# Kernel optimization log

Hardware: AMD Instinct MI355X
Metric: run time of the kernel (lower is better)

Reference implementation:

```python
import jax, jax.numpy as jnp
import numpy as np

GAMMA = 0.5
BATCH, DIM, UNITS = 16384, 512, 1024


def setup_inputs() -> dict:
    key = jax.random.key(0)
    k1, k2 = jax.random.split(key)
    inputs = jax.random.normal(k1, (BATCH, DIM), dtype=jnp.float32)
    mu = jax.random.normal(k2, (DIM, UNITS), dtype=jnp.float32)
    return {"inputs": inputs, "mu": mu}


def reference(inputs, mu):
    # Squared L2 distance from each input row to each center (column of mu):
    x_sq = jnp.sum(inputs * inputs, axis=1, keepdims=True)        # [B, 1]
    mu_sq = jnp.sum(mu * mu, axis=0, keepdims=True)               # [1, U]
    cross = inputs @ mu                                           # [B, U] GEMM
    l2 = x_sq - 2.0 * cross + mu_sq                                # [B, U]
    return jnp.exp(-GAMMA * l2)
```

## Files before the change

kernel.cpp:

```cpp
#include <hip/hip_runtime.h>
#include <hip/hip_bf16.h>

#define BATCH 16384
#define DIM   512
#define UNITS 1024

typedef float v16f __attribute__((ext_vector_type(16)));

#define APITCH 516
#define BPITCH 33

#define MFMA_F8(a, b, c) __builtin_amdgcn_mfma_f32_32x32x16_fp8_fp8((a), (b), (c), 0, 0, 0)

__device__ __forceinline__ void async_copy16(const void* g, void* l) {
    __builtin_amdgcn_global_load_lds(
        (const __attribute__((address_space(1))) void*)g,
        (__attribute__((address_space(3))) void*)l,
        16 , 0 , 0 );
}

__global__ __launch_bounds__(256)
void prep_kernel(const float* __restrict__ in, const float* __restrict__ mu,
                 unsigned char* __restrict__ A8f, unsigned char* __restrict__ B8f,
                 float* __restrict__ xsq, float* __restrict__ musq) {
    __shared__ __attribute__((aligned(16))) char smem[512 * BPITCH * 4 + 1024];
    const int t  = threadIdx.x;
    const int l  = t & 63, w = t >> 6;
    const int ln = l & 31, h = l >> 5;

    if (blockIdx.x >= UNITS / 32) {
        float* lds = (float*)smem;
        float* red = (float*)(smem + 32 * APITCH * 4);
        const int bb = blockIdx.x - UNITS / 32;
        const int c  = (bb & 7) * 64 + (bb >> 3);
        const float4* src = (const float4*)(in + (size_t)c * 32 * DIM);
        float4* l4 = (float4*)lds;
#pragma unroll
        for (int i = 0; i < 16; i++) {
            const int f = i * 256 + t;
            l4[(f >> 7) * (APITCH / 4) + (f & 127)] = src[f];
        }
        __syncthreads();
        float s = 0.f;
#pragma unroll
        for (int j = 0; j < 8; j++) {
            const int kw = w * 8 + j;
            const float* p = lds + ln * APITCH + kw * 16 + h * 8;
            float4 f0 = *(const float4*)p;
            float4 f1 = *(const float4*)(p + 4);
            s += f0.x * f0.x + f0.y * f0.y + f0.z * f0.z + f0.w * f0.w
               + f1.x * f1.x + f1.y * f1.y + f1.z * f1.z + f1.w * f1.w;
            int lo = __builtin_amdgcn_cvt_pk_fp8_f32(f0.x, f0.y, 0, false);
            lo     = __builtin_amdgcn_cvt_pk_fp8_f32(f0.z, f0.w, lo, true);
            int hi = __builtin_amdgcn_cvt_pk_fp8_f32(f1.x, f1.y, 0, false);
            hi     = __builtin_amdgcn_cvt_pk_fp8_f32(f1.z, f1.w, hi, true);
            *(int2*)(A8f + (((size_t)c * 32 + kw) * 64 + l) * 8) = make_int2(lo, hi);
        }
        red[ln * 8 + w * 2 + h] = s;
        __syncthreads();
        if (t < 32) {
            float a = 0.f;
#pragma unroll
            for (int i = 0; i < 8; i++) a += red[t * 8 + i];
            xsq[c * 32 + t] = a;
        }
    } else {
        float* lds = (float*)smem;
        float* red = (float*)(smem + 512 * BPITCH * 4);
        const int nb = blockIdx.x;
        const int n0 = nb * 32;
        const int col = t & 31, kg = t >> 5;
        float s = 0.f;
        for (int i = 0; i < 64; i++) {
            const int k = i * 8 + kg;
            float v = mu[(size_t)k * UNITS + n0 + col];
            s += v * v;
            lds[k * BPITCH + col] = v;
        }
        red[col * 8 + kg] = s;
        __syncthreads();
        if (t < 32) {
            float a = 0.f;
#pragma unroll
            for (int i = 0; i < 8; i++) a += red[t * 8 + i];
            musq[n0 + t] = a;
        }
#pragma unroll
        for (int j = 0; j < 8; j++) {
            const int kw = w * 8 + j;
            const float* p = lds + (kw * 16 + h * 8) * BPITCH + ln;
            float f[8];
#pragma unroll
            for (int i = 0; i < 8; i++) f[i] = p[i * BPITCH];
            int lo = __builtin_amdgcn_cvt_pk_fp8_f32(f[0], f[1], 0, false);
            lo     = __builtin_amdgcn_cvt_pk_fp8_f32(f[2], f[3], lo, true);
            int hi = __builtin_amdgcn_cvt_pk_fp8_f32(f[4], f[5], 0, false);
            hi     = __builtin_amdgcn_cvt_pk_fp8_f32(f[6], f[7], hi, true);
            *(int2*)(B8f + (((size_t)nb * 32 + kw) * 64 + l) * 8) = make_int2(lo, hi);
        }
    }
}

__global__ __launch_bounds__(256, 4)
void rbf_gemm_kernel(const unsigned char* __restrict__ A8f,
                     const unsigned char* __restrict__ B8f,
                     const float* __restrict__ xsq,
                     const float* __restrict__ musq,
                     float* __restrict__ out) {
    __shared__ __attribute__((aligned(16))) unsigned char Bs[32768];

    const int t  = threadIdx.x;
    const int l  = t & 63;
    const int w  = t >> 6;
    const int ln = l & 31;
    const int h  = l >> 5;

    const int b   = blockIdx.x;
    const int xcd = b & 7;
    const int j   = b >> 3;
    const int m0  = (xcd * 8 + (j & 7)) * 256;
    const int n0  = (j >> 3) * 64;

    const unsigned char* bsrc = B8f + (size_t)n0 * 512;
#pragma unroll
    for (int i = 0; i < 8; i++) {
        const int c = i * 256 + t;
        async_copy16(bsrc + c * 16, Bs + c * 16);
    }
    __syncthreads();

    const long* BsL = (const long*)Bs;
    const long* Bp  = BsL + l;

#pragma unroll
    for (int p = 0; p < 2; p++) {
        const int mbase = m0 + w * 64 + p * 32;
        const long* Af = (const long*)A8f + (size_t)(mbase >> 5) * 2048 + l;

        v16f acc0 = (v16f)0.f, acc1 = (v16f)0.f;
#pragma unroll 4
        for (int kw = 0; kw < 32; kw++) {
            long a  = Af[kw * 64];
            long b0 = Bp[kw * 64];
            long b1 = Bp[2048 + kw * 64];
            acc0 = MFMA_F8(a, b0, acc0);
            acc1 = MFMA_F8(a, b1, acc1);
        }

        const float xv  = -0.5f * xsq[mbase + ln];
        const float mb0 = -0.5f * musq[n0 + ln];
        const float mb1 = -0.5f * musq[n0 + 32 + ln];
        float* obase = out + n0 + ln;
#pragma unroll
        for (int r = 0; r < 16; r++) {
            const int rl = (r & 3) + 8 * (r >> 2) + 4 * h;
            const float xb = __shfl(xv, rl, 64);
            float* orow = obase + (size_t)(mbase + rl) * UNITS;
            __builtin_nontemporal_store(__expf(acc0[r] + xb + mb0), orow);
            __builtin_nontemporal_store(__expf(acc1[r] + xb + mb1), orow + 32);
        }
    }
}

extern "C" void kernel_launch(void* const* d_in, const int* in_sizes, int n_in,
                              void* d_out, int out_size, void* d_ws, size_t ws_size,
                              hipStream_t stream) {
    const float* inputs = (const float*)d_in[0];
    const float* mu     = (const float*)d_in[1];
    float* out = (float*)d_out;

    char* ws = (char*)d_ws;
    unsigned char* A8f = (unsigned char*)ws;
    unsigned char* B8f = (unsigned char*)(ws + (size_t)BATCH * DIM);
    float* xsq  = (float*)(ws + (size_t)BATCH * DIM + (size_t)UNITS * DIM);
    float* musq = xsq + BATCH;

    prep_kernel<<<UNITS / 32 + BATCH / 32, 256, 0, stream>>>(
        inputs, mu, A8f, B8f, xsq, musq);
    rbf_gemm_kernel<<<1024, 256, 0, stream>>>(A8f, B8f, xsq, musq, out);
}
```

Measured before the change: 109.1 us.

## Fuse input fp8 conversion and row norms into the GEMM kernel

The input quantization and row squared-norm computation move out of the prep kernel and into the main GEMM kernel. Each 1024-thread block stages 64 input rows in LDS, converts them to fp8 fragments and reduces the norms locally. The block then computes all 1024 output columns, reading B fragments straight from global/L2 instead of LDS. This removes the A8f/xsq round trip through global memory and shrinks the prep launch. In exchange the kernel uses a large LDS footprint, runs only 256 blocks, and gives up the async B staging and the XCD-aware block mapping.

```diff
diff --git a/kernel.cpp b/kernel.cpp
--- a/kernel.cpp
+++ b/kernel.cpp
@@ -1,5 +1,4 @@
 #include <hip/hip_runtime.h>
-#include <hip/hip_bf16.h>
 
 #define BATCH 16384
 #define DIM   512
@@ -7,155 +6,141 @@
 
 typedef float v16f __attribute__((ext_vector_type(16)));
 
-#define APITCH 516
 #define BPITCH 33
-
 #define MFMA_F8(a, b, c) __builtin_amdgcn_mfma_f32_32x32x16_fp8_fp8((a), (b), (c), 0, 0, 0)
 
-__device__ __forceinline__ void async_copy16(const void* g, void* l) {
-    __builtin_amdgcn_global_load_lds(
-        (const __attribute__((address_space(1))) void*)g,
-        (__attribute__((address_space(3))) void*)l,
-        16 , 0 , 0 );
+static __device__ __forceinline__ int2 cvt8(const float4 f0, const float4 f1) {
+    int lo = __builtin_amdgcn_cvt_pk_fp8_f32(f0.x, f0.y, 0, false);
+    lo     = __builtin_amdgcn_cvt_pk_fp8_f32(f0.z, f0.w, lo, true);
+    int hi = __builtin_amdgcn_cvt_pk_fp8_f32(f1.x, f1.y, 0, false);
+    hi     = __builtin_amdgcn_cvt_pk_fp8_f32(f1.z, f1.w, hi, true);
+    return make_int2(lo, hi);
+}
+static __device__ __forceinline__ float dot8(const float4 f0, const float4 f1) {
+    return f0.x * f0.x + f0.y * f0.y + f0.z * f0.z + f0.w * f0.w
+         + f1.x * f1.x + f1.y * f1.y + f1.z * f1.z + f1.w * f1.w;
 }
 
 __global__ __launch_bounds__(256)
-void prep_kernel(const float* __restrict__ in, const float* __restrict__ mu,
-                 unsigned char* __restrict__ A8f, unsigned char* __restrict__ B8f,
-                 float* __restrict__ xsq, float* __restrict__ musq) {
+void prep_b_kernel(const float* __restrict__ mu, unsigned char* __restrict__ B8f,
+                   float* __restrict__ musq) {
     __shared__ __attribute__((aligned(16))) char smem[512 * BPITCH * 4 + 1024];
+    float* lds = (float*)smem;
+    float* red = (float*)(smem + 512 * BPITCH * 4);
     const int t  = threadIdx.x;
     const int l  = t & 63, w = t >> 6;
     const int ln = l & 31, h = l >> 5;
-
-    if (blockIdx.x >= UNITS / 32) {
-        float* lds = (float*)smem;
-        float* red = (float*)(smem + 32 * APITCH * 4);
-        const int bb = blockIdx.x - UNITS / 32;
-        const int c  = (bb & 7) * 64 + (bb >> 3);
-        const float4* src = (const float4*)(in + (size_t)c * 32 * DIM);
-        float4* l4 = (float4*)lds;
+    const int nb = blockIdx.x;
+    const int n0 = nb * 32;
+    const int col = t & 31, kg = t >> 5;
+    float s = 0.f;
+    for (int i = 0; i < 64; i++) {
+        const int k = i * 8 + kg;
+        float v = mu[(size_t)k * UNITS + n0 + col];
+        s += v * v;
+        lds[k * BPITCH + col] = v;
+    }
+    red[col * 8 + kg] = s;
+    __syncthreads();
+    if (t < 32) {
+        float a = 0.f;
 #pragma unroll
-        for (int i = 0; i < 16; i++) {
-            const int f = i * 256 + t;
-            l4[(f >> 7) * (APITCH / 4) + (f & 127)] = src[f];
-        }
-        __syncthreads();
-        float s = 0.f;
+        for (int i = 0; i < 8; i++) a += red[t * 8 + i];
+        musq[n0 + t] = a;
+    }
 #pragma unroll
-        for (int j = 0; j < 8; j++) {
-            const int kw = w * 8 + j;
-            const float* p = lds + ln * APITCH + kw * 16 + h * 8;
-            float4 f0 = *(const float4*)p;
-            float4 f1 = *(const float4*)(p + 4);
-            s += f0.x * f0.x + f0.y * f0.y + f0.z * f0.z + f0.w * f0.w
-               + f1.x * f1.x + f1.y * f1.y + f1.z * f1.z + f1.w * f1.w;
-            int lo = __builtin_amdgcn_cvt_pk_fp8_f32(f0.x, f0.y, 0, false);
-            lo     = __builtin_amdgcn_cvt_pk_fp8_f32(f0.z, f0.w, lo, true);
-            int hi = __builtin_amdgcn_cvt_pk_fp8_f32(f1.x, f1.y, 0, false);
-            hi     = __builtin_amdgcn_cvt_pk_fp8_f32(f1.z, f1.w, hi, true);
-            *(int2*)(A8f + (((size_t)c * 32 + kw) * 64 + l) * 8) = make_int2(lo, hi);
-        }
-        red[ln * 8 + w * 2 + h] = s;
-        __syncthreads();
-        if (t < 32) {
-            float a = 0.f;
+    for (int j = 0; j < 8; j++) {
+        const int kw = w * 8 + j;
+        const float* p = lds + (kw * 16 + h * 8) * BPITCH + ln;
+        float f[8];
 #pragma unroll
-            for (int i = 0; i < 8; i++) a += red[t * 8 + i];
-            xsq[c * 32 + t] = a;
-        }
-    } else {
-        float* lds = (float*)smem;
-        float* red = (float*)(smem + 512 * BPITCH * 4);
-        const int nb = blockIdx.x;
-        const int n0 = nb * 32;
-        const int col = t & 31, kg = t >> 5;
-        float s = 0.f;
-        for (int i = 0; i < 64; i++) {
-            const int k = i * 8 + kg;
-            float v = mu[(size_t)k * UNITS + n0 + col];
-            s += v * v;
-            lds[k * BPITCH + col] = v;
-        }
-        red[col * 8 + kg] = s;
-        __syncthreads();
-        if (t < 32) {
-            float a = 0.f;
-#pragma unroll
-            for (int i = 0; i < 8; i++) a += red[t * 8 + i];
-            musq[n0 + t] = a;
-        }
-#pragma unroll
-        for (int j = 0; j < 8; j++) {
-            const int kw = w * 8 + j;
-            const float* p = lds + (kw * 16 + h * 8) * BPITCH + ln;
-            float f[8];
-#pragma unroll
-            for (int i = 0; i < 8; i++) f[i] = p[i * BPITCH];
-            int lo = __builtin_amdgcn_cvt_pk_fp8_f32(f[0], f[1], 0, false);
-            lo     = __builtin_amdgcn_cvt_pk_fp8_f32(f[2], f[3], lo, true);
-            int hi = __builtin_amdgcn_cvt_pk_fp8_f32(f[4], f[5], 0, false);
-            hi     = __builtin_amdgcn_cvt_pk_fp8_f32(f[6], f[7], hi, true);
-            *(int2*)(B8f + (((size_t)nb * 32 + kw) * 64 + l) * 8) = make_int2(lo, hi);
-        }
+        for (int i = 0; i < 8; i++) f[i] = p[i * BPITCH];
+        *(int2*)(B8f + (((size_t)nb * 32 + kw) * 64 + l) * 8) =
+            cvt8(make_float4(f[0], f[1], f[2], f[3]),
+                 make_float4(f[4], f[5], f[6], f[7]));
     }
 }
 
-__global__ __launch_bounds__(256, 4)
-void rbf_gemm_kernel(const unsigned char* __restrict__ A8f,
+__global__ __launch_bounds__(1024, 4)
+void rbf_main_kernel(const float* __restrict__ in,
                      const unsigned char* __restrict__ B8f,
-                     const float* __restrict__ xsq,
                      const float* __restrict__ musq,
                      float* __restrict__ out) {
-    __shared__ __attribute__((aligned(16))) unsigned char Bs[32768];
+    __shared__ __attribute__((aligned(16))) unsigned char smem[107520];
+    float* stage = (float*)smem;
+    unsigned char* Afrag = smem + 66048;
+    float* red   = (float*)(smem + 98816);
+    float* xsq_l = (float*)(smem + 107264);
 
     const int t  = threadIdx.x;
     const int l  = t & 63;
     const int w  = t >> 6;
     const int ln = l & 31;
     const int h  = l >> 5;
+    const int m0 = blockIdx.x * 64;
 
-    const int b   = blockIdx.x;
-    const int xcd = b & 7;
-    const int j   = b >> 3;
-    const int m0  = (xcd * 8 + (j & 7)) * 256;
-    const int n0  = (j >> 3) * 64;
-
-    const unsigned char* bsrc = B8f + (size_t)n0 * 512;
 #pragma unroll
-    for (int i = 0; i < 8; i++) {
-        const int c = i * 256 + t;
-        async_copy16(bsrc + c * 16, Bs + c * 16);
+    for (int rc = 0; rc < 2; rc++) {
+        const float4* src = (const float4*)(in + (size_t)(m0 + rc * 32) * DIM);
+        float4* s4 = (float4*)stage;
+#pragma unroll
+        for (int i = 0; i < 4; i++) {
+            const int f = i * 1024 + t;
+            s4[(f >> 7) * 129 + (f & 127)] = src[f];
+        }
+        __syncthreads();
+        float s = 0.f;
+#pragma unroll
+        for (int j = 0; j < 2; j++) {
+            const int kw = w * 2 + j;
+            const float* p = stage + ln * 516 + kw * 16 + h * 8;
+            float4 f0 = *(const float4*)p;
+            float4 f1 = *(const float4*)(p + 4);
+            s += dot8(f0, f1);
+            *(int2*)(Afrag + (((rc * 32 + kw) * 64) + h * 32 + ln) * 8) =
+                cvt8(f0, f1);
+        }
+        red[(rc * 32 + ln) * 33 + w * 2 + h] = s;
+        __syncthreads();
+    }
+    if (t < 64) {
+        float a = 0.f;
+#pragma unroll
+        for (int i = 0; i < 32; i++) a += red[t * 33 + i];
+        xsq_l[t] = -0.5f * a;
     }
     __syncthreads();
 
-    const long* BsL = (const long*)Bs;
-    const long* Bp  = BsL + l;
+    const int wr = w >> 3;
+    const int wc = w & 7;
+    const long* Af = (const long*)(Afrag + (size_t)wr * 16384);
+    const long* Bg = (const long*)B8f + (size_t)(wc * 4) * 2048 + l;
+    const size_t mrow = m0 + wr * 32;
 
 #pragma unroll
-    for (int p = 0; p < 2; p++) {
-        const int mbase = m0 + w * 64 + p * 32;
-        const long* Af = (const long*)A8f + (size_t)(mbase >> 5) * 2048 + l;
+    for (int g2 = 0; g2 < 2; g2++) {
+        const long* B0 = Bg + (size_t)(g2 * 2) * 2048;
+        const long* B1 = B0 + 2048;
 
         v16f acc0 = (v16f)0.f, acc1 = (v16f)0.f;
-#pragma unroll 4
+#pragma unroll 8
         for (int kw = 0; kw < 32; kw++) {
-            long a  = Af[kw * 64];
-            long b0 = Bp[kw * 64];
-            long b1 = Bp[2048 + kw * 64];
+            long a  = Af[kw * 64 + l];
+            long b0 = B0[kw * 64];
+            long b1 = B1[kw * 64];
             acc0 = MFMA_F8(a, b0, acc0);
             acc1 = MFMA_F8(a, b1, acc1);
         }
 
-        const float xv  = -0.5f * xsq[mbase + ln];
-        const float mb0 = -0.5f * musq[n0 + ln];
-        const float mb1 = -0.5f * musq[n0 + 32 + ln];
-        float* obase = out + n0 + ln;
+        const int nc0 = wc * 128 + g2 * 64;
+        const float mb0 = -0.5f * musq[nc0 + ln];
+        const float mb1 = -0.5f * musq[nc0 + 32 + ln];
+        float* obase = out + nc0 + ln;
 #pragma unroll
         for (int r = 0; r < 16; r++) {
             const int rl = (r & 3) + 8 * (r >> 2) + 4 * h;
-            const float xb = __shfl(xv, rl, 64);
-            float* orow = obase + (size_t)(mbase + rl) * UNITS;
+            const float xb = xsq_l[wr * 32 + rl];
+            float* orow = obase + (mrow + rl) * UNITS;
             __builtin_nontemporal_store(__expf(acc0[r] + xb + mb0), orow);
             __builtin_nontemporal_store(__expf(acc1[r] + xb + mb1), orow + 32);
         }
@@ -170,12 +155,9 @@
     float* out = (float*)d_out;
 
     char* ws = (char*)d_ws;
-    unsigned char* A8f = (unsigned char*)ws;
-    unsigned char* B8f = (unsigned char*)(ws + (size_t)BATCH * DIM);
-    float* xsq  = (float*)(ws + (size_t)BATCH * DIM + (size_t)UNITS * DIM);
-    float* musq = xsq + BATCH;
+    unsigned char* B8f = (unsigned char*)ws;
+    float* musq = (float*)(ws + (size_t)UNITS * DIM);
 
-    prep_kernel<<<UNITS / 32 + BATCH / 32, 256, 0, stream>>>(
-        inputs, mu, A8f, B8f, xsq, musq);
-    rbf_gemm_kernel<<<1024, 256, 0, stream>>>(A8f, B8f, xsq, musq, out);
+    prep_b_kernel<<<32, 256, 0, stream>>>(mu, B8f, musq);
+    rbf_main_kernel<<<256, 1024, 0, stream>>>(inputs, B8f, musq, out);
 }
```

New measurement: 107.7 us. No clear change (-1.3%).
